# Optimization experiments

Hardware: AMD Instinct MI355X
Metric: run time of the kernel (lower is better)

The kernel has to match this reference:

```python
import jax, jax.numpy as jnp
import numpy as np

N = 50000
E = 1600000
IN_C = 512
HID = 64
OUT_C = 64
HEADS = 2
K = 2
NEG_SLOPE = 0.2


def setup_inputs() -> dict:
    key = jax.random.key(0)
    ks = jax.random.split(key, 9)
    x = jax.random.normal(ks[0], (N, IN_C), dtype=jnp.float32)
    edge_index = jax.random.randint(ks[1], (2, E), 0, N, dtype=jnp.int64)
    edge_attr = jax.random.uniform(ks[2], (E,), dtype=jnp.float32)
    # SGConv linear (glorot-ish init)
    W_sg = jax.random.normal(ks[3], (IN_C, HID), dtype=jnp.float32) / np.sqrt(IN_C)
    b_sg = jnp.zeros((HID,), dtype=jnp.float32)
    # GATConv: lin (no bias), attention vectors, output bias (concat=False -> size OUT_C)
    W_gat = jax.random.normal(ks[4], (HID, HEADS * OUT_C), dtype=jnp.float32) / np.sqrt(HID)
    att_src = jax.random.normal(ks[5], (HEADS, OUT_C), dtype=jnp.float32) / np.sqrt(OUT_C)
    att_dst = jax.random.normal(ks[6], (HEADS, OUT_C), dtype=jnp.float32) / np.sqrt(OUT_C)
    b_gat = jnp.zeros((OUT_C,), dtype=jnp.float32)
    return {"x": x, "edge_index": edge_index, "edge_attr": edge_attr,
            "W_sg": W_sg, "b_sg": b_sg, "W_gat": W_gat,
            "att_src": att_src, "att_dst": att_dst, "b_gat": b_gat}


def reference(x, edge_index, edge_attr, W_sg, b_sg, W_gat, att_src, att_dst, b_gat):
    n = x.shape[0]
    src, dst = edge_index[0], edge_index[1]
    # add self-loops (weight 1) once; reused by SGConv (gcn_norm) and GAT
    loop = jnp.arange(n, dtype=src.dtype)
    src2 = jnp.concatenate([src, loop])
    dst2 = jnp.concatenate([dst, loop])
    ew = jnp.concatenate([edge_attr, jnp.ones((n,), x.dtype)])

    # ---- SGConv: K hops of D^-1/2 A D^-1/2, then linear ----
    deg = jax.ops.segment_sum(ew, dst2, num_segments=n)
    dinv = jnp.where(deg > 0, jax.lax.rsqrt(deg), 0.0)
    norm = dinv[src2] * ew * dinv[dst2]  # [E+N]
    h = x
    for _ in range(K):
        h = jax.ops.segment_sum(norm[:, None] * h[src2], dst2, num_segments=n)
    h = h @ W_sg + b_sg  # [N, HID]

    # activation (SELU); dropout is identity in eval mode
    h = jax.nn.selu(h)

    # ---- GATConv (heads, concat=False -> mean over heads) ----
    g = (h @ W_gat).reshape(n, HEADS, OUT_C)  # [N, H, C]
    a_src = jnp.einsum('nhc,hc->nh', g, att_src)  # [N, H]
    a_dst = jnp.einsum('nhc,hc->nh', g, att_dst)
    e = jax.nn.leaky_relu(a_src[src2] + a_dst[dst2], NEG_SLOPE)  # [E+N, H]
    # per-destination softmax (numerically stable)
    emax = jax.ops.segment_max(e, dst2, num_segments=n)
    emax = jnp.where(jnp.isfinite(emax), emax, 0.0)
    ee = jnp.exp(e - emax[dst2])
    denom = jax.ops.segment_sum(ee, dst2, num_segments=n)
    alpha = ee / jnp.maximum(denom[dst2], 1e-16)  # [E+N, H]
    out = jax.ops.segment_sum(alpha[:, :, None] * g[src2], dst2, num_segments=n)  # [N, H, C]
    return out.mean(axis=1) + b_gat  # [N, OUT_C]
```

## Files before the change

### kernel.cpp

```cpp
#include <hip/hip_runtime.h>
#include <hip/hip_fp16.h>
#include <math.h>

#define N_NODES 50000
#define N_EDGES 1600000
#define IN_CH 512
#define HID 64
#define OUTC 64
#define NEG_SLOPE 0.2f
#define EA_SCALE 131072.0f
#define PCAP 128
#define SLOTS 64

typedef __attribute__((ext_vector_type(8))) short bf16x8;
typedef __attribute__((ext_vector_type(4))) float f32x4;

__device__ __forceinline__ unsigned bf16r(float f) {
    unsigned b = __float_as_uint(f);
    return (b + 0x7FFFu + ((b >> 16) & 1u)) >> 16;
}

__device__ __forceinline__ void gload16(const void* g, void* l) {
    __builtin_amdgcn_global_load_lds(
        (const __attribute__((address_space(1))) void*)g,
        (__attribute__((address_space(3))) void*)l, 16, 0, 0);
}

__device__ __forceinline__ float2 h2f2(unsigned u) {
    return __half22float2(*(__half2*)&u);
}

__global__ void k_wsplit(const float* __restrict__ W, short* __restrict__ Wfrag) {
    int idx = blockIdx.x * 256 + threadIdx.x;
    if (idx >= IN_CH * HID) return;
    int k = idx >> 6, c = idx & 63;
    float wv = W[idx];
    unsigned h = bf16r(wv);
    float res = wv - __uint_as_float(h << 16);
    unsigned l = bf16r(res);
    int kstep = k >> 5, cb = c >> 4;
    int lane = (c & 15) | (((k >> 3) & 3) << 4);
    int j = k & 7;
    int base = ((kstep * 4 + cb) * 2) * 512 + lane * 8 + j;
    Wfrag[base] = (short)h;
    Wfrag[base + 512] = (short)l;
}

#define G1R 64
#define G1KC 64
__global__ __launch_bounds__(256) void k_gemm_hist(const float* __restrict__ x,
                                                   const short* __restrict__ Wfrag,
                                                   __half* __restrict__ p,
                                                   const int* __restrict__ src,
                                                   const int* __restrict__ dst,
                                                   const float* __restrict__ ea,
                                                   unsigned* __restrict__ deg32,
                                                   int* __restrict__ edges4) {
    __shared__ float xs[2][G1R][G1KC];
    int tid = threadIdx.x;
    int bid = blockIdx.x;

    if (bid & 1) {
        int e0 = (bid >> 1) * 2048;
        int e1 = e0 + 2048; if (e1 > N_EDGES) e1 = N_EDGES;
        for (int e = e0 + tid; e < e1; e += 256) {
            int d = dst[e];
            float w = ea[e];
            unsigned pack = (1u << 24) | (unsigned)(w * EA_SCALE);
            unsigned old = atomicAdd(&deg32[d], pack);
            int rank = (int)(old >> 24);
            if (rank < SLOTS) {
                int rec = (src[e] << 16) | (int)__half_as_ushort(__float2half_rn(w));
                __builtin_nontemporal_store(rec, &edges4[d * SLOTS + rank]);
            }
        }
        return;
    }

    int lane = tid & 63, wv = tid >> 6;
    int r0 = (bid >> 1) * G1R;
    f32x4 acc0 = {0.f, 0.f, 0.f, 0.f};
    f32x4 acc1 = {0.f, 0.f, 0.f, 0.f};
    f32x4 acc2 = {0.f, 0.f, 0.f, 0.f};
    f32x4 acc3 = {0.f, 0.f, 0.f, 0.f};

    auto stage = [&](int b, int k0) {
#pragma unroll
        for (int it = 0; it < 4; it++) {
            int rowbase = it * 16 + wv * 4;
            int row = rowbase + (lane >> 4);
            int gr = r0 + row; if (gr > N_NODES - 1) gr = N_NODES - 1;
            int col = ((lane & 15) ^ (row & 7)) << 2;
            gload16(x + (size_t)gr * IN_CH + k0 + col, &xs[b][rowbase][0]);
        }
    };

    stage(0, 0);
    asm volatile("s_waitcnt vmcnt(0)" ::: "memory");
    __syncthreads();

    int cur = 0;
    int arow = wv * 16 + (lane & 15);
    const char* xsbase = (const char*)&xs[0][0][0];
    for (int k0 = 0; k0 < IN_CH; k0 += G1KC) {
        if (k0 + G1KC < IN_CH) stage(cur ^ 1, k0 + G1KC);
#pragma unroll
        for (int kk = 0; kk < 2; kk++) {
            int ks = (k0 >> 5) + kk;
            const short* wb = Wfrag + ks * 4096 + (lane << 3);
            bf16x8 bh0 = *(const bf16x8*)(wb);
            bf16x8 bl0 = *(const bf16x8*)(wb + 512);
            bf16x8 bh1 = *(const bf16x8*)(wb + 1024);
            bf16x8 bl1 = *(const bf16x8*)(wb + 1536);
            bf16x8 bh2 = *(const bf16x8*)(wb + 2048);
            bf16x8 bl2 = *(const bf16x8*)(wb + 2560);
            bf16x8 bh3 = *(const bf16x8*)(wb + 3072);
            bf16x8 bl3 = *(const bf16x8*)(wb + 3584);
            int c16 = kk * 8 + ((lane >> 4) << 1);
            size_t rb = (size_t)cur * (G1R * G1KC * 4) + (size_t)arow * (G1KC * 4);
            float4 xa = *(const float4*)(xsbase + rb + (((c16    ) ^ (arow & 7)) << 4));
            float4 xb = *(const float4*)(xsbase + rb + (((c16 + 1) ^ (arow & 7)) << 4));
            float xv[8] = {xa.x, xa.y, xa.z, xa.w, xb.x, xb.y, xb.z, xb.w};
            bf16x8 ah, al;
#pragma unroll
            for (int j = 0; j < 8; j++) {
                unsigned b = __float_as_uint(xv[j]);
                float res = xv[j] - __uint_as_float(b & 0xFFFF0000u);
                ah[j] = (short)(b >> 16);
                al[j] = (short)(__float_as_uint(res) >> 16);
            }
            acc0 = __builtin_amdgcn_mfma_f32_16x16x32_bf16(ah, bh0, acc0, 0, 0, 0);
            acc0 = __builtin_amdgcn_mfma_f32_16x16x32_bf16(ah, bl0, acc0, 0, 0, 0);
            acc0 = __builtin_amdgcn_mfma_f32_16x16x32_bf16(al, bh0, acc0, 0, 0, 0);
            acc1 = __builtin_amdgcn_mfma_f32_16x16x32_bf16(ah, bh1, acc1, 0, 0, 0);
            acc1 = __builtin_amdgcn_mfma_f32_16x16x32_bf16(ah, bl1, acc1, 0, 0, 0);
            acc1 = __builtin_amdgcn_mfma_f32_16x16x32_bf16(al, bh1, acc1, 0, 0, 0);
            acc2 = __builtin_amdgcn_mfma_f32_16x16x32_bf16(ah, bh2, acc2, 0, 0, 0);
            acc2 = __builtin_amdgcn_mfma_f32_16x16x32_bf16(ah, bl2, acc2, 0, 0, 0);
            acc2 = __builtin_amdgcn_mfma_f32_16x16x32_bf16(al, bh2, acc2, 0, 0, 0);
            acc3 = __builtin_amdgcn_mfma_f32_16x16x32_bf16(ah, bh3, acc3, 0, 0, 0);
            acc3 = __builtin_amdgcn_mfma_f32_16x16x32_bf16(ah, bl3, acc3, 0, 0, 0);
            acc3 = __builtin_amdgcn_mfma_f32_16x16x32_bf16(al, bh3, acc3, 0, 0, 0);
        }
        asm volatile("s_waitcnt vmcnt(0)" ::: "memory");
        __syncthreads();
        cur ^= 1;
    }
    int crow = r0 + wv * 16 + ((lane >> 4) << 2);
    int ccol = lane & 15;
#pragma unroll
    for (int r = 0; r < 4; r++) {
        int gr = crow + r;
        if (gr < N_NODES) {
            p[(unsigned)gr * HID + ccol]      = __float2half(acc0[r]);
            p[(unsigned)gr * HID + 16 + ccol] = __float2half(acc1[r]);
            p[(unsigned)gr * HID + 32 + ccol] = __float2half(acc2[r]);
            p[(unsigned)gr * HID + 48 + ccol] = __float2half(acc3[r]);
        }
    }
}

__global__ void k_hscale(unsigned* __restrict__ h2, const unsigned* __restrict__ deg32,
                         float* __restrict__ dinv) {
    int idx = blockIdx.x * 256 + threadIdx.x;
    if (idx >= N_NODES * 32) return;
    int v = idx >> 5;
    float dv = rsqrtf(1.0f + (float)(deg32[v] & 0xFFFFFFu) * (1.0f / EA_SCALE));
    if ((idx & 31) == 0) dinv[v] = dv;
    unsigned u = h2[idx];
    float2 f = h2f2(u);
    __half2 r = __floats2half2_rn(f.x * dv, f.y * dv);
    h2[idx] = *(unsigned*)&r;
}

__global__ __launch_bounds__(256) void k_hop(const uint2* __restrict__ hin4,
                                             const unsigned* __restrict__ deg32,
                                             const int* __restrict__ edges4,
                                             const float* __restrict__ dinv,
                                             uint2* __restrict__ hout4,
                                             int pw) {
    __shared__ float4 part[2][16];
    int tid = threadIdx.x;
    int w = tid >> 6, lane = tid & 63;
    int slot = w >> 1, half = w & 1;
    int cl = lane & 15, es = lane >> 4;
    int v = blockIdx.x * 2 + slot;
    int cnt = (int)(deg32[v] >> 24);
    if (cnt > SLOTS) cnt = SLOTS;
    int beg = v * SLOTS, end = beg + cnt;
    int mid = beg + (cnt >> 1);
    int lo = half ? mid : beg;
    int hi = half ? end : mid;
    float a0 = 0.f, a1 = 0.f, a2 = 0.f, a3 = 0.f;
    float b0 = 0.f, b1 = 0.f, b2 = 0.f, b3 = 0.f;
    float c0 = 0.f, c1 = 0.f, c2 = 0.f, c3 = 0.f;
    float d0 = 0.f, d1 = 0.f, d2 = 0.f, d3 = 0.f;
    if (!half && !es) {
        uint2 u = hin4[(unsigned)v * 16 + cl];
        float2 f0 = h2f2(u.x), f1 = h2f2(u.y);
        a0 = f0.x; a1 = f0.y; a2 = f1.x; a3 = f1.y;
    }
    int i = lo;
    for (; i + 16 <= hi; i += 16) {
        int r0 = edges4[i + es];
        int r1 = edges4[i + 4 + es];
        int r2 = edges4[i + 8 + es];
        int r3 = edges4[i + 12 + es];
        uint2 g0 = hin4[(((unsigned)r0 >> 16) << 4) + cl];
        uint2 g1 = hin4[(((unsigned)r1 >> 16) << 4) + cl];
        uint2 g2 = hin4[(((unsigned)r2 >> 16) << 4) + cl];
        uint2 g3 = hin4[(((unsigned)r3 >> 16) << 4) + cl];
        float w0 = __half2float(__ushort_as_half((unsigned short)(r0 & 0xFFFF)));
        float w1 = __half2float(__ushort_as_half((unsigned short)(r1 & 0xFFFF)));
        float w2 = __half2float(__ushort_as_half((unsigned short)(r2 & 0xFFFF)));
        float w3 = __half2float(__ushort_as_half((unsigned short)(r3 & 0xFFFF)));
        float2 g0a = h2f2(g0.x), g0b = h2f2(g0.y);
        float2 g1a = h2f2(g1.x), g1b = h2f2(g1.y);
        float2 g2a = h2f2(g2.x), g2b = h2f2(g2.y);
        float2 g3a = h2f2(g3.x), g3b = h2f2(g3.y);
        a0 += w0 * g0a.x; a1 += w0 * g0a.y; a2 += w0 * g0b.x; a3 += w0 * g0b.y;
        b0 += w1 * g1a.x; b1 += w1 * g1a.y; b2 += w1 * g1b.x; b3 += w1 * g1b.y;
        c0 += w2 * g2a.x; c1 += w2 * g2a.y; c2 += w2 * g2b.x; c3 += w2 * g2b.y;
        d0 += w3 * g3a.x; d1 += w3 * g3a.y; d2 += w3 * g3b.x; d3 += w3 * g3b.y;
    }
    for (; i + 8 <= hi; i += 8) {
        int r0 = edges4[i + es];
        int r1 = edges4[i + 4 + es];
        uint2 g0 = hin4[(((unsigned)r0 >> 16) << 4) + cl];
        uint2 g1 = hin4[(((unsigned)r1 >> 16) << 4) + cl];
        float w0 = __half2float(__ushort_as_half((unsigned short)(r0 & 0xFFFF)));
        float w1 = __half2float(__ushort_as_half((unsigned short)(r1 & 0xFFFF)));
        float2 g0a = h2f2(g0.x), g0b = h2f2(g0.y);
        float2 g1a = h2f2(g1.x), g1b = h2f2(g1.y);
        a0 += w0 * g0a.x; a1 += w0 * g0a.y; a2 += w0 * g0b.x; a3 += w0 * g0b.y;
        b0 += w1 * g1a.x; b1 += w1 * g1a.y; b2 += w1 * g1b.x; b3 += w1 * g1b.y;
    }
    for (; i + es < hi; i += 4) {
        int r0 = edges4[i + es];
        uint2 g0 = hin4[(((unsigned)r0 >> 16) << 4) + cl];
        float w0 = __half2float(__ushort_as_half((unsigned short)(r0 & 0xFFFF)));
        float2 g0a = h2f2(g0.x), g0b = h2f2(g0.y);
        a0 += w0 * g0a.x; a1 += w0 * g0a.y; a2 += w0 * g0b.x; a3 += w0 * g0b.y;
    }
    a0 += b0 + c0 + d0; a1 += b1 + c1 + d1;
    a2 += b2 + c2 + d2; a3 += b3 + c3 + d3;
    a0 += __shfl_xor(a0, 16); a1 += __shfl_xor(a1, 16);
    a2 += __shfl_xor(a2, 16); a3 += __shfl_xor(a3, 16);
    a0 += __shfl_xor(a0, 32); a1 += __shfl_xor(a1, 32);
    a2 += __shfl_xor(a2, 32); a3 += __shfl_xor(a3, 32);
    if (half && lane < 16) part[slot][cl] = make_float4(a0, a1, a2, a3);
    __syncthreads();
    if (!half && lane < 16) {
        float dv = dinv[v];
        float sc = (pw == 2) ? dv * dv : dv;
        float4 pp = part[slot][cl];
        __half2 h0 = __floats2half2_rn(sc * (a0 + pp.x), sc * (a1 + pp.y));
        __half2 h1 = __floats2half2_rn(sc * (a2 + pp.z), sc * (a3 + pp.w));
        hout4[(unsigned)v * 16 + cl] = make_uint2(*(unsigned*)&h0, *(unsigned*)&h1);
    }
}

#define G2_ROWS 32
__global__ __launch_bounds__(256) void k_act_gemm2(const __half* __restrict__ h2,
                                                   const float* __restrict__ bsg,
                                                   const float* __restrict__ Wg,
                                                   const float* __restrict__ att_s,
                                                   const float* __restrict__ att_d,
                                                   uint2* __restrict__ g4h,
                                                   float2* __restrict__ asrc2,
                                                   float4* __restrict__ admm) {
    __shared__ float hs[G2_ROWS][HID];
    int tid = threadIdx.x;
    int wave = tid >> 6, lane = tid & 63;
    int r0 = blockIdx.x * G2_ROWS;
    int rbase = wave * 8;

    const float SC = 1.0507009873554805f, AL = 1.6732632423543772f;
    {
        int row = tid >> 3, c0 = (tid & 7) * 8;
        int r = r0 + row;
        float vals[8];
        if (r < N_NODES) {
            uint4 raw = *(const uint4*)(h2 + (unsigned)r * HID + c0);
            float2 f0 = h2f2(raw.x), f1 = h2f2(raw.y), f2 = h2f2(raw.z), f3 = h2f2(raw.w);
            vals[0] = f0.x; vals[1] = f0.y; vals[2] = f1.x; vals[3] = f1.y;
            vals[4] = f2.x; vals[5] = f2.y; vals[6] = f3.x; vals[7] = f3.y;
        } else {
#pragma unroll
            for (int j = 0; j < 8; j++) vals[j] = 0.f;
        }
#pragma unroll
        for (int j = 0; j < 8; j++) {
            float hv = vals[j] + bsg[c0 + j];
            hv = (hv > 0.f) ? SC * hv : SC * AL * (__expf(hv) - 1.f);
            hs[row][c0 + j] = hv;
        }
    }
    __syncthreads();

    float accx[8], accy[8];
#pragma unroll
    for (int j = 0; j < 8; j++) { accx[j] = 0.f; accy[j] = 0.f; }
#pragma unroll 2
    for (int k = 0; k < HID; k++) {
        float w0 = Wg[(size_t)k * 128 + lane];
        float w1 = Wg[(size_t)k * 128 + 64 + lane];
#pragma unroll
        for (int j = 0; j < 8; j++) {
            float hk = hs[rbase + j][k];
            accx[j] += hk * w0;
            accy[j] += hk * w1;
        }
    }
    float ats0 = att_s[lane], ats1 = att_s[64 + lane];
    float atd0 = att_d[lane], atd1 = att_d[64 + lane];
#pragma unroll
    for (int j = 0; j < 8; j++) {
        int v = r0 + rbase + j;
        if (v >= N_NODES) break;
        __half2 gp = __floats2half2_rn(accx[j], accy[j]);
        unsigned gpu = *(unsigned*)&gp;
        unsigned other = (unsigned)__shfl_xor((int)gpu, 1);
        if (!(lane & 1)) g4h[(unsigned)v * 32 + (lane >> 1)] = make_uint2(gpu, other);
        float s0 = accx[j] * ats0, s1 = accy[j] * ats1;
        float d0 = accx[j] * atd0, d1 = accy[j] * atd1;
#pragma unroll
        for (int o = 32; o > 0; o >>= 1) {
            s0 += __shfl_xor(s0, o);
            s1 += __shfl_xor(s1, o);
            d0 += __shfl_xor(d0, o);
            d1 += __shfl_xor(d1, o);
        }
        if (lane == 0) {
            asrc2[v] = make_float2(s0, s1);
            float m0 = s0 + d0; m0 = (m0 > 0.f) ? m0 : NEG_SLOPE * m0;
            float m1 = s1 + d1; m1 = (m1 > 0.f) ? m1 : NEG_SLOPE * m1;
            admm[v] = make_float4(d0, d1, m0, m1);
        }
    }
}

__global__ __launch_bounds__(256) void k_gat(const uint2* __restrict__ g4h,
                                             const float2* __restrict__ asrc2,
                                             const float4* __restrict__ admm,
                                             const unsigned* __restrict__ deg32,
                                             const int* __restrict__ edges4,
                                             const float* __restrict__ bgat,
                                             float* __restrict__ out) {
    __shared__ int4 pbuf[2][2][PCAP];
    __shared__ float4 pacc[2][32];
    __shared__ float2 pden[2][32];
    int tid = threadIdx.x;
    int w = tid >> 6, lane = tid & 63;
    int slot = w >> 1, half = w & 1;
    int cl = lane & 31, es = lane >> 5;
    int v = blockIdx.x * 2 + slot;
    float4 am = admm[v];
    int cnt = (int)(deg32[v] >> 24);
    if (cnt > SLOTS) cnt = SLOTS;
    int beg = v * SLOTS, end = beg + cnt;
    int mid = beg + (cnt >> 1);
    int lo = half ? mid : beg;
    int hi = half ? end : mid;
    int n = hi - lo;

    float pd0 = 0.f, pd1 = 0.f;
    for (int i = lo + lane; i < hi; i += 64) {
        int r = edges4[i];
        unsigned s = (unsigned)r >> 16;
        float2 a = asrc2[s];
        float t0 = a.x + am.x; t0 = (t0 > 0.f) ? t0 : NEG_SLOPE * t0;
        float t1 = a.y + am.y; t1 = (t1 > 0.f) ? t1 : NEG_SLOPE * t1;
        float p0 = __expf(t0 - am.z);
        float p1 = __expf(t1 - am.w);
        int idx = i - lo;
        if (idx < PCAP)
            pbuf[slot][half][idx] = make_int4((int)(s << 5), __float_as_int(p0), __float_as_int(p1), 0);
        pd0 += p0; pd1 += p1;
    }
#pragma unroll
    for (int o = 32; o > 0; o >>= 1) {
        pd0 += __shfl_xor(pd0, o);
        pd1 += __shfl_xor(pd1, o);
    }
    if (!half) { pd0 += 1.f; pd1 += 1.f; }

    float aA = 0.f, aB = 0.f, aC = 0.f, aD = 0.f;
    float bA = 0.f, bB = 0.f, bC = 0.f, bD = 0.f;
    if (!half && !es) {
        uint2 gs = g4h[(unsigned)v * 32 + cl];
        float2 gx = h2f2(gs.x), gy = h2f2(gs.y);
        aA = gx.x; aB = gx.y; aC = gy.x; aD = gy.y;
    }
    int ii = 0;
    for (; ii + 8 <= n; ii += 8) {
        int4 e0 = pbuf[slot][half][ii + es];
        int4 e1 = pbuf[slot][half][ii + 2 + es];
        int4 e2 = pbuf[slot][half][ii + 4 + es];
        int4 e3 = pbuf[slot][half][ii + 6 + es];
        uint2 g0 = g4h[(unsigned)(e0.x + cl)];
        uint2 g1 = g4h[(unsigned)(e1.x + cl)];
        uint2 g2 = g4h[(unsigned)(e2.x + cl)];
        uint2 g3 = g4h[(unsigned)(e3.x + cl)];
        float p00 = __int_as_float(e0.y), p01 = __int_as_float(e0.z);
        float p10 = __int_as_float(e1.y), p11 = __int_as_float(e1.z);
        float p20 = __int_as_float(e2.y), p21 = __int_as_float(e2.z);
        float p30 = __int_as_float(e3.y), p31 = __int_as_float(e3.z);
        float2 g0x = h2f2(g0.x), g0y = h2f2(g0.y);
        float2 g1x = h2f2(g1.x), g1y = h2f2(g1.y);
        float2 g2x = h2f2(g2.x), g2y = h2f2(g2.y);
        float2 g3x = h2f2(g3.x), g3y = h2f2(g3.y);
        aA += p00 * g0x.x; aB += p01 * g0x.y; aC += p00 * g0y.x; aD += p01 * g0y.y;
        bA += p10 * g1x.x; bB += p11 * g1x.y; bC += p10 * g1y.x; bD += p11 * g1y.y;
        aA += p20 * g2x.x; aB += p21 * g2x.y; aC += p20 * g2y.x; aD += p21 * g2y.y;
        bA += p30 * g3x.x; bB += p31 * g3x.y; bC += p30 * g3y.x; bD += p31 * g3y.y;
    }
    for (; ii + es < n; ii += 2) {
        int4 e0 = pbuf[slot][half][ii + es];
        uint2 g0 = g4h[(unsigned)(e0.x + cl)];
        float p00 = __int_as_float(e0.y), p01 = __int_as_float(e0.z);
        float2 g0x = h2f2(g0.x), g0y = h2f2(g0.y);
        aA += p00 * g0x.x; aB += p01 * g0x.y; aC += p00 * g0y.x; aD += p01 * g0y.y;
    }
    aA += bA; aB += bB; aC += bC; aD += bD;
    aA += __shfl_xor(aA, 32); aB += __shfl_xor(aB, 32);
    aC += __shfl_xor(aC, 32); aD += __shfl_xor(aD, 32);
    if (half && lane < 32) {
        pacc[slot][cl] = make_float4(aA, aB, aC, aD);
        pden[slot][cl] = make_float2(pd0, pd1);
    }
    __syncthreads();
    if (!half && lane < 32) {
        float4 pa = pacc[slot][cl];
        float2 pd = pden[slot][cl];
        float r0 = 1.f / (pd0 + pd.x), r1 = 1.f / (pd1 + pd.y);
        float oe = 0.5f * ((aA + pa.x) * r0 + (aB + pa.y) * r1) + bgat[cl * 2];
        float oo = 0.5f * ((aC + pa.z) * r0 + (aD + pa.w) * r1) + bgat[cl * 2 + 1];
        *(float2*)&out[(unsigned)v * OUTC + cl * 2] = make_float2(oe, oo);
    }
}

extern "C" void kernel_launch(void* const* d_in, const int* in_sizes, int n_in,
                              void* d_out, int out_size, void* d_ws, size_t ws_size,
                              hipStream_t stream) {
    const float* x     = (const float*)d_in[0];
    const int*   ei    = (const int*)d_in[1];
    const float* ea    = (const float*)d_in[2];
    const float* Wsg   = (const float*)d_in[3];
    const float* bsg   = (const float*)d_in[4];
    const float* Wg    = (const float*)d_in[5];
    const float* att_s = (const float*)d_in[6];
    const float* att_d = (const float*)d_in[7];
    const float* bgat  = (const float*)d_in[8];
    const int* src = ei;
    const int* dst = ei + N_EDGES;
    float* out = (float*)d_out;

    char* ws = (char*)d_ws;
    size_t off = 0;
    auto alloc = [&](size_t bytes) -> void* {
        void* p = ws + off;
        off = (off + bytes + 255) & ~(size_t)255;
        return p;
    };
    unsigned* deg32  = (unsigned*)alloc((size_t)N_NODES * 4);
    float*    dinv   = (float*)alloc((size_t)N_NODES * 4);
    int*      edges4 = (int*)alloc((size_t)N_NODES * SLOTS * 4);
    short*    Wfrag  = (short*)alloc((size_t)IN_CH * HID * 2 * 2);
    __half*   h0     = (__half*)alloc((size_t)N_NODES * HID * 2);
    __half*   h1     = (__half*)alloc((size_t)N_NODES * HID * 2);
    uint2*    g4h    = (uint2*)alloc((size_t)N_NODES * 32 * 8);
    float2*   asrc2  = (float2*)alloc((size_t)N_NODES * 8);
    float4*   admm   = (float4*)alloc((size_t)N_NODES * 16);
    (void)ws_size; (void)in_sizes; (void)n_in; (void)out_size;

    hipMemsetAsync(deg32, 0, (size_t)N_NODES * 4, stream);

    k_wsplit<<<(IN_CH * HID + 255) / 256, 256, 0, stream>>>(Wsg, Wfrag);

    k_gemm_hist<<<1564, 256, 0, stream>>>(x, Wfrag, h0, src, dst, ea, deg32, edges4);

    k_hscale<<<(N_NODES * 32 + 255) / 256, 256, 0, stream>>>((unsigned*)h0, deg32, dinv);

    k_hop<<<N_NODES / 2, 256, 0, stream>>>((const uint2*)h0, deg32, edges4, dinv, (uint2*)h1, 2);
    k_hop<<<N_NODES / 2, 256, 0, stream>>>((const uint2*)h1, deg32, edges4, dinv, (uint2*)h0, 1);
    k_act_gemm2<<<(N_NODES + G2_ROWS - 1) / G2_ROWS, 256, 0, stream>>>(h0, bsg, Wg, att_s, att_d, g4h, asrc2, admm);
    k_gat<<<N_NODES / 2, 256, 0, stream>>>(g4h, asrc2, admm, deg32, edges4, bgat, out);
}
```

Before: 280.3 us.

## Replace fixed-slot atomic edge bucketing with two-pass radix-partitioned exact CSR build

```diff
diff --git a/kernel.cpp b/kernel.cpp
--- a/kernel.cpp
+++ b/kernel.cpp
@@ -10,7 +10,9 @@
 #define NEG_SLOPE 0.2f
 #define EA_SCALE 131072.0f
 #define PCAP 128
-#define SLOTS 64
+#define NBUCK 196
+#define NB1 782
+#define NSCAN (NBUCK * NB1)
 
 typedef __attribute__((ext_vector_type(8))) short bf16x8;
 typedef __attribute__((ext_vector_type(4))) float f32x4;
@@ -48,32 +50,27 @@
 
 #define G1R 64
 #define G1KC 64
-__global__ __launch_bounds__(256) void k_gemm_hist(const float* __restrict__ x,
-                                                   const short* __restrict__ Wfrag,
-                                                   __half* __restrict__ p,
-                                                   const int* __restrict__ src,
-                                                   const int* __restrict__ dst,
-                                                   const float* __restrict__ ea,
-                                                   unsigned* __restrict__ deg32,
-                                                   int* __restrict__ edges4) {
+__global__ __launch_bounds__(256) void k_gemm_p1a(const float* __restrict__ x,
+                                                  const short* __restrict__ Wfrag,
+                                                  __half* __restrict__ p,
+                                                  const int* __restrict__ dst,
+                                                  int* __restrict__ gh) {
     __shared__ float xs[2][G1R][G1KC];
+    __shared__ int hist[NBUCK];
     int tid = threadIdx.x;
     int bid = blockIdx.x;
 
     if (bid & 1) {
-        int e0 = (bid >> 1) * 2048;
+        int blk = bid >> 1;
+        for (int j = tid; j < NBUCK; j += 256) hist[j] = 0;
+        __syncthreads();
+        int e0 = blk * 2048;
         int e1 = e0 + 2048; if (e1 > N_EDGES) e1 = N_EDGES;
-        for (int e = e0 + tid; e < e1; e += 256) {
-            int d = dst[e];
-            float w = ea[e];
-            unsigned pack = (1u << 24) | (unsigned)(w * EA_SCALE);
-            unsigned old = atomicAdd(&deg32[d], pack);
-            int rank = (int)(old >> 24);
-            if (rank < SLOTS) {
-                int rec = (src[e] << 16) | (int)__half_as_ushort(__float2half_rn(w));
-                __builtin_nontemporal_store(rec, &edges4[d * SLOTS + rank]);
-            }
-        }
+        for (int e = e0 + tid; e < e1; e += 256)
+            atomicAdd(&hist[((unsigned)dst[e]) >> 8], 1);
+        __syncthreads();
+        for (int j = tid; j < NBUCK; j += 256)
+            gh[j * NB1 + blk] = hist[j];
         return;
     }
 
@@ -160,13 +157,138 @@
     }
 }
 
-__global__ void k_hscale(unsigned* __restrict__ h2, const unsigned* __restrict__ deg32,
-                         float* __restrict__ dinv) {
+__global__ void k_scan_reduce(const int* __restrict__ counts, int* bsum, int n) {
+    __shared__ int lds[256];
+    int i = blockIdx.x * 256 + threadIdx.x;
+    lds[threadIdx.x] = (i < n) ? counts[i] : 0;
+    __syncthreads();
+    for (int s = 128; s > 0; s >>= 1) {
+        if (threadIdx.x < s) lds[threadIdx.x] += lds[threadIdx.x + s];
+        __syncthreads();
+    }
+    if (threadIdx.x == 0) bsum[blockIdx.x] = lds[0];
+}
+
+__global__ void k_scan_mid(int* bsum, int nb) {
+    __shared__ int lds[256];
+    __shared__ int carry;
+    int t = threadIdx.x;
+    if (t == 0) carry = 0;
+    __syncthreads();
+    for (int base = 0; base < nb; base += 256) {
+        int i = base + t;
+        int v = (i < nb) ? bsum[i] : 0;
+        int orig = v;
+        lds[t] = v;
+        __syncthreads();
+        for (int s = 1; s < 256; s <<= 1) {
+            int add = (t >= s) ? lds[t - s] : 0;
+            __syncthreads();
+            lds[t] += add;
+            __syncthreads();
+        }
+        int c = carry;
+        if (i < nb) bsum[i] = lds[t] - orig + c;
+        __syncthreads();
+        if (t == 0) carry = c + lds[255];
+        __syncthreads();
+    }
+}
+
+__global__ void k_scan_final(const int* __restrict__ counts, const int* __restrict__ bsum,
+                             int* __restrict__ outx, int n) {
+    __shared__ int lds[256];
+    int t = threadIdx.x;
+    int i = blockIdx.x * 256 + t;
+    int v = (i < n) ? counts[i] : 0;
+    lds[t] = v;
+    __syncthreads();
+    for (int s = 1; s < 256; s <<= 1) {
+        int add = (t >= s) ? lds[t - s] : 0;
+        __syncthreads();
+        lds[t] += add;
+        __syncthreads();
+    }
+    if (i < n) outx[i] = bsum[blockIdx.x] + lds[t] - v;
+}
+
+__global__ __launch_bounds__(256) void k_p1b(const int* __restrict__ src,
+                                             const int* __restrict__ dst,
+                                             const float* __restrict__ ea,
+                                             const int* __restrict__ ghs,
+                                             int2* __restrict__ part) {
+    __shared__ int curb[NBUCK];
+    int tid = threadIdx.x;
+    int blk = blockIdx.x;
+    for (int j = tid; j < NBUCK; j += 256) curb[j] = ghs[j * NB1 + blk];
+    __syncthreads();
+    int e0 = blk * 2048;
+    int e1 = e0 + 2048; if (e1 > N_EDGES) e1 = N_EDGES;
+    for (int e = e0 + tid; e < e1; e += 256) {
+        int s = src[e], d = dst[e];
+        unsigned eb = __float_as_uint(ea[e]);
+        int b = ((unsigned)d) >> 8;
+        int pos = atomicAdd(&curb[b], 1);
+        part[pos] = make_int2((s << 16) | (int)(eb & 0xFFFFu),
+                              d | (int)(eb & 0xFFFF0000u));
+    }
+}
+
+__global__ __launch_bounds__(256) void k_p2(const int2* __restrict__ part,
+                                            const int* __restrict__ ghs,
+                                            int* __restrict__ offs,
+                                            float* __restrict__ dinv,
+                                            int* __restrict__ edges4) {
+    __shared__ int cnt[256];
+    __shared__ unsigned degs[256];
+    __shared__ int sc[256];
+    int tid = threadIdx.x;
+    int b = blockIdx.x;
+    int vb = b << 8;
+    int bs = ghs[b * NB1];
+    int be = (b == NBUCK - 1) ? N_EDGES : ghs[(b + 1) * NB1];
+    cnt[tid] = 0; degs[tid] = 0u;
+    __syncthreads();
+    for (int i = bs + tid; i < be; i += 256) {
+        int2 r = part[i];
+        int idx = r.y & 255;
+        unsigned eb = ((unsigned)r.y & 0xFFFF0000u) | ((unsigned)r.x & 0xFFFFu);
+        atomicAdd(&cnt[idx], 1);
+        atomicAdd(&degs[idx], (unsigned)(__uint_as_float(eb) * EA_SCALE));
+    }
+    __syncthreads();
+    sc[tid] = cnt[tid];
+    __syncthreads();
+    for (int s = 1; s < 256; s <<= 1) {
+        int add = (tid >= s) ? sc[tid - s] : 0;
+        __syncthreads();
+        sc[tid] += add;
+        __syncthreads();
+    }
+    int excl = sc[tid] - cnt[tid];
+    int v = vb + tid;
+    if (v < N_NODES) {
+        offs[v] = bs + excl;
+        dinv[v] = rsqrtf(1.0f + (float)degs[tid] * (1.0f / EA_SCALE));
+    }
+    cnt[tid] = bs + excl;
+    __syncthreads();
+    for (int i = bs + tid; i < be; i += 256) {
+        int2 r = part[i];
+        int idx = r.y & 255;
+        unsigned eb = ((unsigned)r.y & 0xFFFF0000u) | ((unsigned)r.x & 0xFFFFu);
+        int pos = atomicAdd(&cnt[idx], 1);
+        int srec = (int)((unsigned)r.x >> 16);
+        edges4[pos] = (srec << 16) |
+                      (int)__half_as_ushort(__float2half_rn(__uint_as_float(eb)));
+    }
+    if (b == 0 && tid == 0) offs[N_NODES] = N_EDGES;
+}
+
+__global__ void k_hscale(unsigned* __restrict__ h2, const float* __restrict__ dinv) {
     int idx = blockIdx.x * 256 + threadIdx.x;
     if (idx >= N_NODES * 32) return;
-    int v = idx >> 5;
-    float dv = rsqrtf(1.0f + (float)(deg32[v] & 0xFFFFFFu) * (1.0f / EA_SCALE));
-    if ((idx & 31) == 0) dinv[v] = dv;
+    float dv = dinv[idx >> 5];
     unsigned u = h2[idx];
     float2 f = h2f2(u);
     __half2 r = __floats2half2_rn(f.x * dv, f.y * dv);
@@ -174,7 +296,7 @@
 }
 
 __global__ __launch_bounds__(256) void k_hop(const uint2* __restrict__ hin4,
-                                             const unsigned* __restrict__ deg32,
+                                             const int* __restrict__ offs,
                                              const int* __restrict__ edges4,
                                              const float* __restrict__ dinv,
                                              uint2* __restrict__ hout4,
@@ -185,44 +307,19 @@
     int slot = w >> 1, half = w & 1;
     int cl = lane & 15, es = lane >> 4;
     int v = blockIdx.x * 2 + slot;
-    int cnt = (int)(deg32[v] >> 24);
-    if (cnt > SLOTS) cnt = SLOTS;
-    int beg = v * SLOTS, end = beg + cnt;
+    int beg = offs[v], end = offs[v + 1];
+    int cnt = end - beg;
     int mid = beg + (cnt >> 1);
     int lo = half ? mid : beg;
     int hi = half ? end : mid;
     float a0 = 0.f, a1 = 0.f, a2 = 0.f, a3 = 0.f;
     float b0 = 0.f, b1 = 0.f, b2 = 0.f, b3 = 0.f;
-    float c0 = 0.f, c1 = 0.f, c2 = 0.f, c3 = 0.f;
-    float d0 = 0.f, d1 = 0.f, d2 = 0.f, d3 = 0.f;
     if (!half && !es) {
         uint2 u = hin4[(unsigned)v * 16 + cl];
         float2 f0 = h2f2(u.x), f1 = h2f2(u.y);
         a0 = f0.x; a1 = f0.y; a2 = f1.x; a3 = f1.y;
     }
     int i = lo;
-    for (; i + 16 <= hi; i += 16) {
-        int r0 = edges4[i + es];
-        int r1 = edges4[i + 4 + es];
-        int r2 = edges4[i + 8 + es];
-        int r3 = edges4[i + 12 + es];
-        uint2 g0 = hin4[(((unsigned)r0 >> 16) << 4) + cl];
-        uint2 g1 = hin4[(((unsigned)r1 >> 16) << 4) + cl];
-        uint2 g2 = hin4[(((unsigned)r2 >> 16) << 4) + cl];
-        uint2 g3 = hin4[(((unsigned)r3 >> 16) << 4) + cl];
-        float w0 = __half2float(__ushort_as_half((unsigned short)(r0 & 0xFFFF)));
-        float w1 = __half2float(__ushort_as_half((unsigned short)(r1 & 0xFFFF)));
-        float w2 = __half2float(__ushort_as_half((unsigned short)(r2 & 0xFFFF)));
-        float w3 = __half2float(__ushort_as_half((unsigned short)(r3 & 0xFFFF)));
-        float2 g0a = h2f2(g0.x), g0b = h2f2(g0.y);
-        float2 g1a = h2f2(g1.x), g1b = h2f2(g1.y);
-        float2 g2a = h2f2(g2.x), g2b = h2f2(g2.y);
-        float2 g3a = h2f2(g3.x), g3b = h2f2(g3.y);
-        a0 += w0 * g0a.x; a1 += w0 * g0a.y; a2 += w0 * g0b.x; a3 += w0 * g0b.y;
-        b0 += w1 * g1a.x; b1 += w1 * g1a.y; b2 += w1 * g1b.x; b3 += w1 * g1b.y;
-        c0 += w2 * g2a.x; c1 += w2 * g2a.y; c2 += w2 * g2b.x; c3 += w2 * g2b.y;
-        d0 += w3 * g3a.x; d1 += w3 * g3a.y; d2 += w3 * g3b.x; d3 += w3 * g3b.y;
-    }
     for (; i + 8 <= hi; i += 8) {
         int r0 = edges4[i + es];
         int r1 = edges4[i + 4 + es];
@@ -242,8 +339,7 @@
         float2 g0a = h2f2(g0.x), g0b = h2f2(g0.y);
         a0 += w0 * g0a.x; a1 += w0 * g0a.y; a2 += w0 * g0b.x; a3 += w0 * g0b.y;
     }
-    a0 += b0 + c0 + d0; a1 += b1 + c1 + d1;
-    a2 += b2 + c2 + d2; a3 += b3 + c3 + d3;
+    a0 += b0; a1 += b1; a2 += b2; a3 += b3;
     a0 += __shfl_xor(a0, 16); a1 += __shfl_xor(a1, 16);
     a2 += __shfl_xor(a2, 16); a3 += __shfl_xor(a3, 16);
     a0 += __shfl_xor(a0, 32); a1 += __shfl_xor(a1, 32);
@@ -343,7 +439,7 @@
 __global__ __launch_bounds__(256) void k_gat(const uint2* __restrict__ g4h,
                                              const float2* __restrict__ asrc2,
                                              const float4* __restrict__ admm,
-                                             const unsigned* __restrict__ deg32,
+                                             const int* __restrict__ offs,
                                              const int* __restrict__ edges4,
                                              const float* __restrict__ bgat,
                                              float* __restrict__ out) {
@@ -356,9 +452,8 @@
     int cl = lane & 31, es = lane >> 5;
     int v = blockIdx.x * 2 + slot;
     float4 am = admm[v];
-    int cnt = (int)(deg32[v] >> 24);
-    if (cnt > SLOTS) cnt = SLOTS;
-    int beg = v * SLOTS, end = beg + cnt;
+    int beg = offs[v], end = offs[v + 1];
+    int cnt = end - beg;
     int mid = beg + (cnt >> 1);
     int lo = half ? mid : beg;
     int hi = half ? end : mid;
@@ -392,8 +487,9 @@
         float2 gx = h2f2(gs.x), gy = h2f2(gs.y);
         aA = gx.x; aB = gx.y; aC = gy.x; aD = gy.y;
     }
+    int n1 = (n < PCAP) ? n : PCAP;
     int ii = 0;
-    for (; ii + 8 <= n; ii += 8) {
+    for (; ii + 8 <= n1; ii += 8) {
         int4 e0 = pbuf[slot][half][ii + es];
         int4 e1 = pbuf[slot][half][ii + 2 + es];
         int4 e2 = pbuf[slot][half][ii + 4 + es];
@@ -415,12 +511,24 @@
         aA += p20 * g2x.x; aB += p21 * g2x.y; aC += p20 * g2y.x; aD += p21 * g2y.y;
         bA += p30 * g3x.x; bB += p31 * g3x.y; bC += p30 * g3y.x; bD += p31 * g3y.y;
     }
-    for (; ii + es < n; ii += 2) {
+    for (; ii + es < n1; ii += 2) {
         int4 e0 = pbuf[slot][half][ii + es];
         uint2 g0 = g4h[(unsigned)(e0.x + cl)];
         float p00 = __int_as_float(e0.y), p01 = __int_as_float(e0.z);
         float2 g0x = h2f2(g0.x), g0y = h2f2(g0.y);
         aA += p00 * g0x.x; aB += p01 * g0x.y; aC += p00 * g0y.x; aD += p01 * g0y.y;
+    }
+    for (int jj = PCAP + es; jj < n; jj += 2) {
+        int r = edges4[lo + jj];
+        unsigned s = (unsigned)r >> 16;
+        float2 a = asrc2[s];
+        float t0 = a.x + am.x; t0 = (t0 > 0.f) ? t0 : NEG_SLOPE * t0;
+        float t1 = a.y + am.y; t1 = (t1 > 0.f) ? t1 : NEG_SLOPE * t1;
+        float p0 = __expf(t0 - am.z);
+        float p1 = __expf(t1 - am.w);
+        uint2 g0 = g4h[(s << 5) + cl];
+        float2 g0x = h2f2(g0.x), g0y = h2f2(g0.y);
+        aA += p0 * g0x.x; aB += p1 * g0x.y; aC += p0 * g0y.x; aD += p1 * g0y.y;
     }
     aA += bA; aB += bB; aC += bC; aD += bD;
     aA += __shfl_xor(aA, 32); aB += __shfl_xor(aB, 32);
@@ -463,9 +571,13 @@
         off = (off + bytes + 255) & ~(size_t)255;
         return p;
     };
-    unsigned* deg32  = (unsigned*)alloc((size_t)N_NODES * 4);
+    int*      gh     = (int*)alloc((size_t)NSCAN * 4);
+    int*      ghs    = (int*)alloc((size_t)NSCAN * 4);
+    int*      bsum   = (int*)alloc(1024 * 4);
+    int2*     part   = (int2*)alloc((size_t)N_EDGES * 8);
+    int*      edges4 = (int*)alloc((size_t)N_EDGES * 4);
+    int*      offs   = (int*)alloc((size_t)(N_NODES + 1) * 4);
     float*    dinv   = (float*)alloc((size_t)N_NODES * 4);
-    int*      edges4 = (int*)alloc((size_t)N_NODES * SLOTS * 4);
     short*    Wfrag  = (short*)alloc((size_t)IN_CH * HID * 2 * 2);
     __half*   h0     = (__half*)alloc((size_t)N_NODES * HID * 2);
     __half*   h1     = (__half*)alloc((size_t)N_NODES * HID * 2);
@@ -474,16 +586,22 @@
     float4*   admm   = (float4*)alloc((size_t)N_NODES * 16);
     (void)ws_size; (void)in_sizes; (void)n_in; (void)out_size;
 
-    hipMemsetAsync(deg32, 0, (size_t)N_NODES * 4, stream);
-
     k_wsplit<<<(IN_CH * HID + 255) / 256, 256, 0, stream>>>(Wsg, Wfrag);
 
-    k_gemm_hist<<<1564, 256, 0, stream>>>(x, Wfrag, h0, src, dst, ea, deg32, edges4);
-
-    k_hscale<<<(N_NODES * 32 + 255) / 256, 256, 0, stream>>>((unsigned*)h0, deg32, dinv);
-
-    k_hop<<<N_NODES / 2, 256, 0, stream>>>((const uint2*)h0, deg32, edges4, dinv, (uint2*)h1, 2);
-    k_hop<<<N_NODES / 2, 256, 0, stream>>>((const uint2*)h1, deg32, edges4, dinv, (uint2*)h0, 1);
+    k_gemm_p1a<<<2 * NB1, 256, 0, stream>>>(x, Wfrag, h0, dst, gh);
+
+    int nb = (NSCAN + 255) / 256;
+    k_scan_reduce<<<nb, 256, 0, stream>>>(gh, bsum, NSCAN);
+    k_scan_mid<<<1, 256, 0, stream>>>(bsum, nb);
+    k_scan_final<<<nb, 256, 0, stream>>>(gh, bsum, ghs, NSCAN);
+
+    k_p1b<<<NB1, 256, 0, stream>>>(src, dst, ea, ghs, part);
+    k_p2<<<NBUCK, 256, 0, stream>>>(part, ghs, offs, dinv, edges4);
+
+    k_hscale<<<(N_NODES * 32 + 255) / 256, 256, 0, stream>>>((unsigned*)h0, dinv);
+
+    k_hop<<<N_NODES / 2, 256, 0, stream>>>((const uint2*)h0, offs, edges4, dinv, (uint2*)h1, 2);
+    k_hop<<<N_NODES / 2, 256, 0, stream>>>((const uint2*)h1, offs, edges4, dinv, (uint2*)h0, 1);
     k_act_gemm2<<<(N_NODES + G2_ROWS - 1) / G2_ROWS, 256, 0, stream>>>(h0, bsg, Wg, att_s, att_d, g4h, asrc2, admm);
-    k_gat<<<N_NODES / 2, 256, 0, stream>>>(g4h, asrc2, admm, deg32, edges4, bgat, out);
-}
+    k_gat<<<N_NODES / 2, 256, 0, stream>>>(g4h, asrc2, admm, offs, edges4, bgat, out);
+}
```

New measurement: 285.8 us. About the same (+2.0%).
